# Optimization experiments

Measured on AMD Instinct MI355X. Metric: run time of the kernel, lower is better.

The kernel has to match this reference:

```python
import jax, jax.numpy as jnp
import numpy as np

N, E, D, H, G = 100000, 1600000, 128, 256, 64
N0, N1 = 50000, 25000
SLOPE = 0.01  # PyTorch LeakyReLU default


def lrelu(x):
    return jax.nn.leaky_relu(x, SLOPE)


def seg_sum(x, idx, n):
    return jax.ops.segment_sum(x, idx, num_segments=n)


def seg_max(x, idx, n):
    m = jax.ops.segment_max(x, idx, num_segments=n)
    return jnp.where(jnp.isneginf(m), jnp.zeros_like(m), m)


def mpnn(x, edge_index, edge_attr, w1, b1, g, be, w2, b2):
    # MPNN.forward: add_self_loops -> node MLP -> sym-normalized, edge-weighted scatter-add
    n = x.shape[0]
    ar = jnp.arange(n)
    row = jnp.concatenate([edge_index[0], ar])  # source j (x_j gathered here)
    col = jnp.concatenate([edge_index[1], ar])  # target i (aggregation index)
    ea = jnp.concatenate([edge_attr, jnp.ones((n,), x.dtype)])  # self-loop fill=1.0
    # Linear -> BatchNorm1d(eval: mean0/var1) -> Dropout(eval: id) -> LeakyReLU -> Linear
    h = lrelu((x @ w1.T + b1) * g + be) @ w2.T + b2
    deg = seg_sum(jnp.ones(row.shape, x.dtype), row, n)
    dis = jnp.where(deg > 0, deg ** -0.5, 0.0)
    norm = dis[row] * dis[col]
    msg = (norm * ea)[:, None] * h[row]  # gather + elementwise weighting
    return seg_sum(msg, col, n)          # scatter-add aggregation


def _forward(x, edge_attr, energy, params, edge_index, batch, cluster0, cluster1):
    (w0a, b0a, g0, be0, w0b, b0b,
     w1a, b1a, g1, be1, w1b, b1b,
     w2a, b2a, g2, be2, w2b, b2b,
     emb_w, emb_b, emb_g, emb_be,
     lw1, lb1, lg, lbe, lw2, lb2) = params
    h = mpnn(x, edge_index, edge_attr, w0a, b0a, g0, be0, w0b, b0b) + x
    # --- first graclus max_pool (cluster0 precomputed; edges mapped w/o coalesce) ---
    px = seg_max(lrelu(h), cluster0, N0)
    ox = seg_max(x, cluster0, N0)  # max_pool(origin)
    pe = cluster0[edge_index]
    pb = jnp.maximum(jax.ops.segment_max(batch, cluster0, num_segments=N0), 0)
    # NOTE: mpnn_1 output is assigned to a local `x` and discarded in the original forward,
    # so it does not affect the result; we skip the dead computation.
    h2 = px + ox
    # --- second graclus max_pool ---
    px2 = seg_max(lrelu(h2), cluster1, N1)
    pe2 = cluster1[pe]
    pb2 = jnp.maximum(jax.ops.segment_max(pb, cluster1, num_segments=N1), 0)
    h3 = lrelu(mpnn(px2, pe2, edge_attr, w2a, b2a, g2, be2, w2b, b2b))
    gx = seg_max(h3, pb2, G)  # global_max_pool
    e = lrelu((energy.reshape(G, 21) @ emb_w.T + emb_b) * emb_g + emb_be)
    z = jnp.concatenate([gx, e], axis=1)  # [G, D+8]
    z = lrelu((z @ lw1.T + lb1) * lg + lbe)
    return z @ lw2.T + lb2  # [G, 1]


def setup_inputs() -> dict:
    key = jax.random.key(0)
    ks = iter(jax.random.split(key, 40))

    def lin(k, fo, fi):  # kaiming_normal_ fan_in, leaky_relu
        return jax.random.normal(k, (fo, fi), jnp.float32) * np.float32(np.sqrt(2.0 / fi))

    def bias(n):
        return jnp.full((n,), 0.01, jnp.float32)

    inp = {}
    inp['x'] = jax.random.normal(next(ks), (N, D), jnp.float32)
    inp['edge_attr'] = jax.random.uniform(next(ks), (E,), jnp.float32)
    inp['energy'] = jax.random.normal(next(ks), (G * 21,), jnp.float32)
    # mpnn_0 (D->D->D)
    inp['w0a'] = lin(next(ks), D, D); inp['b0a'] = bias(D)
    inp['g0'] = jnp.ones((D,), jnp.float32); inp['be0'] = jnp.zeros((D,), jnp.float32)
    inp['w0b'] = lin(next(ks), D, D); inp['b0b'] = bias(D)
    # mpnn_1 (D->D->D)  (dead in forward, kept as params)
    inp['w1a'] = lin(next(ks), D, D); inp['b1a'] = bias(D)
    inp['g1'] = jnp.ones((D,), jnp.float32); inp['be1'] = jnp.zeros((D,), jnp.float32)
    inp['w1b'] = lin(next(ks), D, D); inp['b1b'] = bias(D)
    # mpnn_2 (D->H->D)
    inp['w2a'] = lin(next(ks), H, D); inp['b2a'] = bias(H)
    inp['g2'] = jnp.ones((H,), jnp.float32); inp['be2'] = jnp.zeros((H,), jnp.float32)
    inp['w2b'] = lin(next(ks), D, H); inp['b2b'] = bias(D)
    # emb (21->8)
    inp['emb_w'] = lin(next(ks), 8, 21); inp['emb_b'] = bias(8)
    inp['emb_g'] = jnp.ones((8,), jnp.float32); inp['emb_be'] = jnp.zeros((8,), jnp.float32)
    # head ((D+8)->D->1)
    inp['lw1'] = lin(next(ks), D, D + 8); inp['lb1'] = bias(D)
    inp['lg'] = jnp.ones((D,), jnp.float32); inp['lbe'] = jnp.zeros((D,), jnp.float32)
    inp['lw2'] = lin(next(ks), 1, D); inp['lb2'] = bias(1)
    # int inputs
    inp['edge_index'] = jax.random.randint(next(ks), (2, E), 0, N, dtype=jnp.int32)
    inp['batch'] = jnp.sort(jax.random.randint(next(ks), (N,), 0, G, dtype=jnp.int32))
    inp['cluster0'] = jax.random.randint(next(ks), (N,), 0, N0, dtype=jnp.int32)
    inp['cluster1'] = jax.random.randint(next(ks), (N0,), 0, N1, dtype=jnp.int32)
    return inp


def reference(x, edge_attr, energy,
              w0a, b0a, g0, be0, w0b, b0b,
              w1a, b1a, g1, be1, w1b, b1b,
              w2a, b2a, g2, be2, w2b, b2b,
              emb_w, emb_b, emb_g, emb_be,
              lw1, lb1, lg, lbe, lw2, lb2,
              edge_index, batch, cluster0, cluster1):
    params = (w0a, b0a, g0, be0, w0b, b0b,
              w1a, b1a, g1, be1, w1b, b1b,
              w2a, b2a, g2, be2, w2b, b2b,
              emb_w, emb_b, emb_g, emb_be,
              lw1, lb1, lg, lbe, lw2, lb2)
    return _forward(x, edge_attr, energy, params, edge_index, batch, cluster0, cluster1)
```

## Files before the change

### kernel.cpp

```cpp
#include <hip/hip_runtime.h>
#include <math.h>

#define N_NODES 100000
#define N_EDGES 1600000
#define DIM     128
#define NPOOL0  50000
#define NPOOL1  25000
#define NGRAPH  64

typedef __attribute__((ext_vector_type(8))) short short8;
typedef __attribute__((ext_vector_type(4))) float f32x4;

__device__ __forceinline__ float lrelu(float v) { return v > 0.f ? v : 0.01f * v; }

__device__ __forceinline__ unsigned short f2bf(float f) {
    unsigned u = __float_as_uint(f);
    unsigned r = u + 0x7FFFu + ((u >> 16) & 1u);
    return (unsigned short)(r >> 16);
}

__device__ __forceinline__ void atomicMaxF(float* addr, float val) {
    if (val >= 0.f) atomicMax((int*)addr, __float_as_int(val));
    else            atomicMin((unsigned int*)addr, __float_as_uint(val));
}

__global__ __launch_bounds__(256) void init_f(float* __restrict__ deg0, float* __restrict__ deg2,
                                              float* __restrict__ gmax) {
    int i = blockIdx.x * 256 + threadIdx.x;
    if (i < N_NODES) deg0[i] = 1.0f;
    else if (i < N_NODES + NPOOL1) deg2[i - N_NODES] = 1.0f;
    else if (i < N_NODES + NPOOL1 + NGRAPH * DIM) gmax[i - N_NODES - NPOOL1] = -INFINITY;
}
__global__ __launch_bounds__(256) void conv_weights(
        const float* __restrict__ w0a, const float* __restrict__ w0b,
        const float* __restrict__ w2a, const float* __restrict__ w2b,
        unsigned short* __restrict__ o0a, unsigned short* __restrict__ o0b,
        unsigned short* __restrict__ o2a, unsigned short* __restrict__ o2b) {
    int i = blockIdx.x * 256 + threadIdx.x;
    if (i < 16384) o0a[i] = f2bf(w0a[i]);
    else if (i < 32768) o0b[i - 16384] = f2bf(w0b[i - 16384]);
    else if (i < 65536) o2a[i - 32768] = f2bf(w2a[i - 32768]);
    else if (i < 98304) o2b[i - 65536] = f2bf(w2b[i - 65536]);
}

template<int KIN, int HID, bool BF16IN>
__global__ __launch_bounds__(256) void mlp_mfma(
        const void* __restrict__ Xv, int R,
        const unsigned short* __restrict__ W1, const float* __restrict__ B1,
        const float* __restrict__ G1, const float* __restrict__ BE1,
        const unsigned short* __restrict__ W2, const float* __restrict__ B2,
        unsigned short* __restrict__ Y)
{
    constexpr int XS_S = KIN + 8;
    constexpr int TS_S = HID + 8;
    __shared__ unsigned short xs[64 * XS_S];
    __shared__ unsigned short ts[64 * TS_S];

    const int tid = threadIdx.x;
    const int r0 = blockIdx.x * 64;

    {
        const int row = tid >> 2;
        const int c0 = (tid & 3) * 32;
        const int gr = r0 + row;
        if (BF16IN) {
            const unsigned short* X = (const unsigned short*)Xv;
            #pragma unroll
            for (int q = 0; q < 4; ++q) {
                short8 v = short8{0,0,0,0,0,0,0,0};
                if (gr < R) v = *(const short8*)&X[(size_t)gr * KIN + c0 + q * 8];
                *(short8*)&xs[row * XS_S + c0 + q * 8] = v;
            }
        } else {
            const float* X = (const float*)Xv;
            #pragma unroll
            for (int q = 0; q < 4; ++q) {
                short8 v = short8{0,0,0,0,0,0,0,0};
                if (gr < R) {
                    float4 a = *(const float4*)&X[(size_t)gr * KIN + c0 + q * 8];
                    float4 b = *(const float4*)&X[(size_t)gr * KIN + c0 + q * 8 + 4];
                    v[0] = (short)f2bf(a.x); v[1] = (short)f2bf(a.y);
                    v[2] = (short)f2bf(a.z); v[3] = (short)f2bf(a.w);
                    v[4] = (short)f2bf(b.x); v[5] = (short)f2bf(b.y);
                    v[6] = (short)f2bf(b.z); v[7] = (short)f2bf(b.w);
                }
                *(short8*)&xs[row * XS_S + c0 + q * 8] = v;
            }
        }
    }
    __syncthreads();

    const int wv = tid >> 6;
    const int lane = tid & 63;
    const int lr = lane & 15;
    const int lq = lane >> 4;
    const int arow = wv * 16 + lr;

    constexpr int NCG1 = HID / 16;
    constexpr int NK1 = KIN / 32;
    f32x4 acc1[NCG1] = {};
    for (int kc = 0; kc < NK1; ++kc) {
        short8 a = *(short8*)&xs[arow * XS_S + kc * 32 + lq * 8];
        #pragma unroll
        for (int cg = 0; cg < NCG1; ++cg) {
            short8 b = *(const short8*)&W1[(size_t)(cg * 16 + lr) * KIN + kc * 32 + lq * 8];
            acc1[cg] = __builtin_amdgcn_mfma_f32_16x16x32_bf16(a, b, acc1[cg], 0, 0, 0);
        }
    }
    #pragma unroll
    for (int cg = 0; cg < NCG1; ++cg) {
        const int c = cg * 16 + lr;
        const float bb = B1[c], gg = G1[c], ee = BE1[c];
        #pragma unroll
        for (int q = 0; q < 4; ++q) {
            const int rr = wv * 16 + lq * 4 + q;
            float v = (acc1[cg][q] + bb) * gg + ee;
            ts[rr * TS_S + c] = f2bf(lrelu(v));
        }
    }

    constexpr int NK2 = HID / 32;
    f32x4 acc2[8] = {};
    for (int kc = 0; kc < NK2; ++kc) {
        short8 a = *(short8*)&ts[arow * TS_S + kc * 32 + lq * 8];
        #pragma unroll
        for (int cg = 0; cg < 8; ++cg) {
            short8 b = *(const short8*)&W2[(size_t)(cg * 16 + lr) * HID + kc * 32 + lq * 8];
            acc2[cg] = __builtin_amdgcn_mfma_f32_16x16x32_bf16(a, b, acc2[cg], 0, 0, 0);
        }
    }
    #pragma unroll
    for (int cg = 0; cg < 8; ++cg) {
        const int c = cg * 16 + lr;
        const float bb = B2[c];
        #pragma unroll
        for (int q = 0; q < 4; ++q) {
            const int gr = r0 + wv * 16 + lq * 4 + q;
            if (gr < R) Y[(size_t)gr * 128 + c] = f2bf(acc2[cg][q] + bb);
        }
    }
}

__global__ __launch_bounds__(256) void count0(const int* __restrict__ src, const int* __restrict__ dst,
                                              float* __restrict__ deg, int* __restrict__ cnt, int E) {
    int e = blockIdx.x * 256 + threadIdx.x;
    if (e < E) {
        atomicAdd(&deg[src[e]], 1.0f);
        atomicAdd(&cnt[dst[e]], 1);
    }
}
__global__ __launch_bounds__(256) void rsqrt_ip(float* __restrict__ p, int n) {
    int i = blockIdx.x * 256 + threadIdx.x;
    if (i < n) p[i] = rsqrtf(p[i]);
}
__global__ __launch_bounds__(256) void mapnode(
        const int* __restrict__ c0, const int* __restrict__ c1,
        const float* __restrict__ deg0, const int* __restrict__ cnt0,
        int* __restrict__ cmap, float* __restrict__ deg2, int* __restrict__ cnt2, int n) {
    int i = blockIdx.x * 256 + threadIdx.x;
    if (i < n) {
        int m = c1[c0[i]];
        cmap[i] = m;
        float oc = deg0[i] - 1.0f;
        if (oc != 0.f) atomicAdd(&deg2[m], oc);
        int ic = cnt0[i];
        if (ic) atomicAdd(&cnt2[m], ic);
    }
}
__global__ __launch_bounds__(256) void scan_blk(const int* __restrict__ cnt, int* __restrict__ offs,
                                                int* __restrict__ bsum, int n) {
    __shared__ int s[256];
    const int tid = threadIdx.x;
    const int i = blockIdx.x * 256 + tid;
    int v = (i < n) ? cnt[i] : 0;
    s[tid] = v;
    __syncthreads();
    #pragma unroll
    for (int d = 1; d < 256; d <<= 1) {
        int t = (tid >= d) ? s[tid - d] : 0;
        __syncthreads();
        s[tid] += t;
        __syncthreads();
    }
    if (i < n) offs[i] = s[tid] - v;
    if (tid == 255) bsum[blockIdx.x] = s[255];
}
__global__ __launch_bounds__(512) void scan_top(int* __restrict__ bsum, int nb) {
    __shared__ int s[512];
    const int tid = threadIdx.x;
    int v = (tid < nb) ? bsum[tid] : 0;
    s[tid] = v;
    __syncthreads();
    #pragma unroll
    for (int d = 1; d < 512; d <<= 1) {
        int t = (tid >= d) ? s[tid - d] : 0;
        __syncthreads();
        s[tid] += t;
        __syncthreads();
    }
    if (tid < nb) bsum[tid] = s[tid] - v;
}
__global__ __launch_bounds__(256) void scan_add(int* __restrict__ offs, const int* __restrict__ bsum,
                                                int* __restrict__ fill, int n) {
    int i = blockIdx.x * 256 + threadIdx.x;
    if (i < n) {
        int o = offs[i] + bsum[i >> 8];
        offs[i] = o;
        fill[i] = o;
    }
}
__global__ __launch_bounds__(256) void place_pack(const int* __restrict__ dst, const int* __restrict__ srcA,
                                                  const float* __restrict__ ea, const float* __restrict__ dis,
                                                  int* __restrict__ fill, int2* __restrict__ pack, int E) {
    int e = blockIdx.x * 256 + threadIdx.x;
    if (e < E) {
        int d = dst[e];
        int s = srcA[e];
        int pos = atomicAdd(&fill[d], 1);
        pack[pos] = make_int2(s, __float_as_int(dis[s] * ea[e]));
    }
}
__global__ __launch_bounds__(256) void edgemap(
        const int* __restrict__ ei0, const int* __restrict__ ei1,
        const int* __restrict__ cmap,
        int* __restrict__ src2, int* __restrict__ dst2, int E)
{
    int e = blockIdx.x * 256 + threadIdx.x;
    if (e < E) {
        src2[e] = cmap[ei0[e]];
        dst2[e] = cmap[ei1[e]];
    }
}
__global__ __launch_bounds__(256) void seg_count(const int* __restrict__ map, int* __restrict__ cnt, int n) {
    int i = blockIdx.x * 256 + threadIdx.x;
    if (i < n) atomicAdd(&cnt[map[i]], 1);
}
__global__ __launch_bounds__(256) void place_idx(const int* __restrict__ map, int* __restrict__ fill,
                                                 int* __restrict__ list, int n) {
    int i = blockIdx.x * 256 + threadIdx.x;
    if (i < n) {
        int pos = atomicAdd(&fill[map[i]], 1);
        list[pos] = i;
    }
}
__global__ __launch_bounds__(256) void segmax_i32(const int* __restrict__ map, const int* __restrict__ vals,
                                                  int* __restrict__ out, int n) {
    int i = blockIdx.x * 256 + threadIdx.x;
    if (i < n) atomicMax(&out[map[i]], vals[i]);
}

#define EDGE_ITER(K, A0, A1) {                                                  \
    int s_ = __builtin_amdgcn_readlane(pv.x, (K));                              \
    float w_ = __int_as_float(__builtin_amdgcn_readlane(pv.y, (K)));            \
    unsigned hv_ = hrows[(size_t)s_ * 64 + lane];                               \
    float c_ = w_ * di;                                                         \
    A0 += c_ * __uint_as_float(hv_ << 16);                                      \
    A1 += c_ * __uint_as_float(hv_ & 0xFFFF0000u); }

__global__ __launch_bounds__(256) void gather0(
        const unsigned short* __restrict__ h16, const float* __restrict__ x,
        const float* __restrict__ dis, const int* __restrict__ offs,
        const int* __restrict__ cnt, const int2* __restrict__ pack,
        unsigned* __restrict__ agg0)
{
    const int wid = (blockIdx.x * 256 + threadIdx.x) >> 6;
    if (wid >= N_NODES) return;
    const int lane = threadIdx.x & 63;
    const float di = dis[wid];
    const unsigned* hrows = (const unsigned*)h16;

    unsigned hself = hrows[(size_t)wid * 64 + lane];
    float a0 = di * di * __uint_as_float(hself << 16);
    float a1 = di * di * __uint_as_float(hself & 0xFFFF0000u);
    float b0 = 0.f, b1 = 0.f;

    const int base = offs[wid], n = cnt[wid];
    int k0 = 0;
    for (; k0 + 64 <= n; k0 += 64) {
        int2 pv = pack[base + k0 + lane];
        #pragma unroll
        for (int k = 0; k < 64; k += 2) {
            EDGE_ITER(k,     a0, a1);
            EDGE_ITER(k + 1, b0, b1);
        }
    }
    const int rem = n - k0;
    if (rem > 0) {
        int2 pv = (lane < rem) ? pack[base + k0 + lane] : make_int2(0, 0);
        #pragma unroll 4
        for (int k = 0; k < rem; ++k) EDGE_ITER(k, a0, a1);
    }
    a0 += b0; a1 += b1;

    float2 xv = *(const float2*)&x[(size_t)wid * DIM + lane * 2];
    agg0[(size_t)wid * 64 + lane] =
        ((unsigned)f2bf(a1 + xv.y) << 16) | (unsigned)f2bf(a0 + xv.x);
}

__global__ __launch_bounds__(256) void gather2(
        const unsigned short* __restrict__ hm2,
        const float* __restrict__ dis, const int* __restrict__ offs,
        const int* __restrict__ cnt, const int2* __restrict__ pack,
        float* __restrict__ agg2)
{
    const int wid = (blockIdx.x * 256 + threadIdx.x) >> 6;
    if (wid >= NPOOL1) return;
    const int lane = threadIdx.x & 63;
    const float di = dis[wid];
    const unsigned* hrows = (const unsigned*)hm2;

    unsigned hself = hrows[(size_t)wid * 64 + lane];
    float a0 = di * di * __uint_as_float(hself << 16);
    float a1 = di * di * __uint_as_float(hself & 0xFFFF0000u);
    float b0 = 0.f, b1 = 0.f;

    const int base = offs[wid], n = cnt[wid];
    int k0 = 0;
    for (; k0 + 64 <= n; k0 += 64) {
        int2 pv = pack[base + k0 + lane];
        #pragma unroll
        for (int k = 0; k < 64; k += 2) {
            EDGE_ITER(k,     a0, a1);
            EDGE_ITER(k + 1, b0, b1);
        }
    }
    const int rem = n - k0;
    if (rem > 0) {
        int2 pv = (lane < rem) ? pack[base + k0 + lane] : make_int2(0, 0);
        #pragma unroll 4
        for (int k = 0; k < rem; ++k) EDGE_ITER(k, a0, a1);
    }
    a0 += b0; a1 += b1;

    float2 o = make_float2(lrelu(a0), lrelu(a1));
    *(float2*)&agg2[(size_t)wid * DIM + lane * 2] = o;
}

__global__ __launch_bounds__(256) void pool1_gather(
        const unsigned* __restrict__ agg0, const float* __restrict__ x,
        const int* __restrict__ offsc, const int* __restrict__ cntc,
        const int* __restrict__ listc, unsigned* __restrict__ h2)
{
    const int c = (blockIdx.x * 256 + threadIdx.x) >> 6;
    if (c >= NPOOL0) return;
    const int lane = threadIdx.x & 63;
    const int base = offsc[c], n = cntc[c];
    float p0 = -INFINITY, p1 = -INFINITY, o0 = -INFINITY, o1 = -INFINITY;
    for (int k = 0; k < n; ++k) {
        const int node = listc[base + k];
        const unsigned hv = agg0[(size_t)node * 64 + lane];
        const float2 xv = *(const float2*)&x[(size_t)node * 128 + lane * 2];
        p0 = fmaxf(p0, lrelu(__uint_as_float(hv << 16)));
        p1 = fmaxf(p1, lrelu(__uint_as_float(hv & 0xFFFF0000u)));
        o0 = fmaxf(o0, xv.x);
        o1 = fmaxf(o1, xv.y);
    }
    p0 = (p0 == -INFINITY) ? 0.f : p0;
    p1 = (p1 == -INFINITY) ? 0.f : p1;
    o0 = (o0 == -INFINITY) ? 0.f : o0;
    o1 = (o1 == -INFINITY) ? 0.f : o1;
    h2[(size_t)c * 64 + lane] =
        ((unsigned)f2bf(p1 + o1) << 16) | (unsigned)f2bf(p0 + o0);
}

__global__ __launch_bounds__(256) void pool2_gather(
        const unsigned* __restrict__ h2,
        const int* __restrict__ offsd, const int* __restrict__ cntd,
        const int* __restrict__ listd, unsigned* __restrict__ x2)
{
    const int d = (blockIdx.x * 256 + threadIdx.x) >> 6;
    if (d >= NPOOL1) return;
    const int lane = threadIdx.x & 63;
    const int base = offsd[d], n = cntd[d];
    float m0 = -INFINITY, m1 = -INFINITY;
    for (int k = 0; k < n; ++k) {
        const int node = listd[base + k];
        const unsigned hv = h2[(size_t)node * 64 + lane];
        m0 = fmaxf(m0, lrelu(__uint_as_float(hv << 16)));
        m1 = fmaxf(m1, lrelu(__uint_as_float(hv & 0xFFFF0000u)));
    }
    m0 = (m0 == -INFINITY) ? 0.f : m0;
    m1 = (m1 == -INFINITY) ? 0.f : m1;
    x2[(size_t)d * 64 + lane] = ((unsigned)f2bf(m1) << 16) | (unsigned)f2bf(m0);
}

__global__ __launch_bounds__(256) void gpool_scan(
        const float* __restrict__ agg2, const int* __restrict__ listg,
        const int* __restrict__ pb2, float* __restrict__ gmax)
{
    const int wave = (blockIdx.x * 256 + threadIdx.x) >> 6;
    const int lane = threadIdx.x & 63;
    const int CH = (NPOOL1 + 511) / 512;
    const int p0 = wave * CH;
    const int p1 = min(p0 + CH, NPOOL1);
    if (p0 >= NPOOL1) return;

    float m0 = -INFINITY, m1 = -INFINITY;
    int cur = -1;
    for (int p = p0; p < p1; ++p) {
        const int node = listg[p];
        const int g = pb2[node];
        if (g != cur) {
            if (cur >= 0) {
                float* gp = &gmax[(size_t)cur * DIM + lane * 2];
                atomicMaxF(gp + 0, m0);
                atomicMaxF(gp + 1, m1);
            }
            cur = g; m0 = -INFINITY; m1 = -INFINITY;
        }
        const float2 v = *(const float2*)&agg2[(size_t)node * DIM + lane * 2];
        m0 = fmaxf(m0, v.x);
        m1 = fmaxf(m1, v.y);
    }
    float* gp = &gmax[(size_t)cur * DIM + lane * 2];
    atomicMaxF(gp + 0, m0);
    atomicMaxF(gp + 1, m1);
}

__global__ __launch_bounds__(128) void head(
        const float* __restrict__ gmax, const float* __restrict__ energy,
        const float* __restrict__ emb_w, const float* __restrict__ emb_b,
        const float* __restrict__ emb_g, const float* __restrict__ emb_be,
        const float* __restrict__ lw1, const float* __restrict__ lb1,
        const float* __restrict__ lg, const float* __restrict__ lbe,
        const float* __restrict__ lw2, const float* __restrict__ lb2,
        float* __restrict__ out)
{
    const int g = blockIdx.x;
    const int t = threadIdx.x;
    __shared__ float z[136];
    __shared__ float red[128];

    {
        float v = gmax[(size_t)g * DIM + t];
        z[t] = (v == -INFINITY) ? 0.f : v;
    }
    if (t < 8) {
        float s = 0.f;
        #pragma unroll
        for (int k = 0; k < 21; ++k) s += energy[g * 21 + k] * emb_w[t * 21 + k];
        s = (s + emb_b[t]) * emb_g[t] + emb_be[t];
        z[128 + t] = lrelu(s);
    }
    __syncthreads();
    float s = 0.f;
    #pragma unroll 8
    for (int k = 0; k < 136; ++k) s += z[k] * lw1[t * 136 + k];
    float z2 = lrelu((s + lb1[t]) * lg[t] + lbe[t]);
    red[t] = z2 * lw2[t];
    __syncthreads();
    if (t == 0) {
        float acc = lb2[0];
        for (int k = 0; k < 128; ++k) acc += red[k];
        out[g] = acc;
    }
}

extern "C" void kernel_launch(void* const* d_in, const int* in_sizes, int n_in,
                              void* d_out, int out_size, void* d_ws, size_t ws_size,
                              hipStream_t stream) {
    const float* x        = (const float*)d_in[0];
    const float* edge_attr= (const float*)d_in[1];
    const float* energy   = (const float*)d_in[2];
    const float* w0a = (const float*)d_in[3];
    const float* b0a = (const float*)d_in[4];
    const float* g0  = (const float*)d_in[5];
    const float* be0 = (const float*)d_in[6];
    const float* w0b = (const float*)d_in[7];
    const float* b0b = (const float*)d_in[8];
    const float* w2a = (const float*)d_in[15];
    const float* b2a = (const float*)d_in[16];
    const float* g2  = (const float*)d_in[17];
    const float* be2 = (const float*)d_in[18];
    const float* w2b = (const float*)d_in[19];
    const float* b2b = (const float*)d_in[20];
    const float* emb_w  = (const float*)d_in[21];
    const float* emb_b  = (const float*)d_in[22];
    const float* emb_g  = (const float*)d_in[23];
    const float* emb_be = (const float*)d_in[24];
    const float* lw1 = (const float*)d_in[25];
    const float* lb1 = (const float*)d_in[26];
    const float* lg  = (const float*)d_in[27];
    const float* lbe = (const float*)d_in[28];
    const float* lw2 = (const float*)d_in[29];
    const float* lb2 = (const float*)d_in[30];
    const int* ei0   = (const int*)d_in[31];
    const int* ei1   = ei0 + N_EDGES;
    const int* batch = (const int*)d_in[32];
    const int* c0    = (const int*)d_in[33];
    const int* c1    = (const int*)d_in[34];
    float* out = (float*)d_out;

    char* ws = (char*)d_ws;
    unsigned short* h16 = (unsigned short*)(ws + 0);
    int*   src2  = (int*)(ws + 0);
    int*   dst2  = (int*)(ws + 6400000);
    float* agg2  = (float*)(ws + 12800000);
    unsigned* agg0 = (unsigned*)(ws + 25600000);
    unsigned short* hm2 = (unsigned short*)(ws + 25600000);
    int2*  pack0 = (int2*)(ws + 51200000);
    int2*  pack2 = (int2*)(ws + 51200000);
    unsigned* h2 = (unsigned*)(ws + 64000000);
    unsigned* x2 = (unsigned*)(ws + 76800000);
    float* deg0  = (float*)(ws + 83200000);
    float* deg2  = (float*)(ws + 83600000);
    char*  zbase = ws + 83700000;
    int*   cnt0  = (int*)(ws + 83700000);
    int*   cnt2  = (int*)(ws + 84100000);
    int*   cntc  = (int*)(ws + 84200000);
    int*   cntd  = (int*)(ws + 84400000);
    int*   cntg  = (int*)(ws + 84500000);
    int*   pb    = (int*)(ws + 84500256);
    int*   pb2   = (int*)(ws + 84700256);
    const size_t ZBYTES = 84800256 - 83700000;
    int*   offs0 = (int*)(ws + 84800256);
    int*   fill0 = (int*)(ws + 85200256);
    int*   offsc = (int*)(ws + 85600256);
    int*   fillc = (int*)(ws + 85800256);
    int*   listc = (int*)(ws + 86000256);
    int*   offsd = (int*)(ws + 86400256);
    int*   filld = (int*)(ws + 86500256);
    int*   listd = (int*)(ws + 86600256);
    int*   offs2 = (int*)(ws + 86800256);
    int*   fill2 = (int*)(ws + 86900256);
    int*   offsg = (int*)(ws + 87000256);
    int*   fillg = (int*)(ws + 87000512);
    int*   listg = (int*)(ws + 87000768);
    int*   bsum  = (int*)(ws + 87100768);
    int*   cmap  = (int*)(ws + 87103000);
    unsigned short* w0a16 = (unsigned short*)(ws + 87503000);
    unsigned short* w0b16 = (unsigned short*)(ws + 87535768);
    unsigned short* w2a16 = (unsigned short*)(ws + 87568536);
    unsigned short* w2b16 = (unsigned short*)(ws + 87634072);
    float* gmax  = (float*)(ws + 87699608);

    (void)in_sizes; (void)n_in; (void)out_size; (void)ws_size;

    const int NB0 = (N_NODES + 255) / 256;
    const int NBC = (NPOOL0 + 255) / 256;
    const int NB1 = (NPOOL1 + 255) / 256;
    const int NBE = (N_EDGES + 255) / 256;

    hipMemsetAsync(zbase, 0, ZBYTES, stream);
    init_f<<<(N_NODES + NPOOL1 + NGRAPH * DIM + 255) / 256, 256, 0, stream>>>(deg0, deg2, gmax);
    conv_weights<<<384, 256, 0, stream>>>(w0a, w0b, w2a, w2b, w0a16, w0b16, w2a16, w2b16);

    mlp_mfma<128, 128, false><<<(N_NODES + 63) / 64, 256, 0, stream>>>(
        x, N_NODES, w0a16, b0a, g0, be0, w0b16, b0b, h16);
    count0<<<NBE, 256, 0, stream>>>(ei0, ei1, deg0, cnt0, N_EDGES);
    mapnode<<<NB0, 256, 0, stream>>>(c0, c1, deg0, cnt0, cmap, deg2, cnt2, N_NODES);
    rsqrt_ip<<<NB0, 256, 0, stream>>>(deg0, N_NODES);
    scan_blk<<<NB0, 256, 0, stream>>>(cnt0, offs0, bsum, N_NODES);
    scan_top<<<1, 512, 0, stream>>>(bsum, NB0);
    scan_add<<<NB0, 256, 0, stream>>>(offs0, bsum, fill0, N_NODES);
    place_pack<<<NBE, 256, 0, stream>>>(ei1, ei0, edge_attr, deg0, fill0, pack0, N_EDGES);
    gather0<<<(N_NODES * 64) / 256, 256, 0, stream>>>(h16, x, deg0, offs0, cnt0, pack0, agg0);

    seg_count<<<NB0, 256, 0, stream>>>(c0, cntc, N_NODES);
    scan_blk<<<NBC, 256, 0, stream>>>(cntc, offsc, bsum, NPOOL0);
    scan_top<<<1, 512, 0, stream>>>(bsum, NBC);
    scan_add<<<NBC, 256, 0, stream>>>(offsc, bsum, fillc, NPOOL0);
    place_idx<<<NB0, 256, 0, stream>>>(c0, fillc, listc, N_NODES);
    segmax_i32<<<NB0, 256, 0, stream>>>(c0, batch, pb, N_NODES);
    pool1_gather<<<(NPOOL0 * 64) / 256, 256, 0, stream>>>(agg0, x, offsc, cntc, listc, h2);

    seg_count<<<NBC, 256, 0, stream>>>(c1, cntd, NPOOL0);
    scan_blk<<<NB1, 256, 0, stream>>>(cntd, offsd, bsum, NPOOL1);
    scan_top<<<1, 512, 0, stream>>>(bsum, NB1);
    scan_add<<<NB1, 256, 0, stream>>>(offsd, bsum, filld, NPOOL1);
    place_idx<<<NBC, 256, 0, stream>>>(c1, filld, listd, NPOOL0);
    segmax_i32<<<NBC, 256, 0, stream>>>(c1, pb, pb2, NPOOL0);
    pool2_gather<<<(NPOOL1 * 64) / 256, 256, 0, stream>>>(h2, offsd, cntd, listd, x2);

    edgemap<<<NBE, 256, 0, stream>>>(ei0, ei1, cmap, src2, dst2, N_EDGES);
    rsqrt_ip<<<NB1, 256, 0, stream>>>(deg2, NPOOL1);
    scan_blk<<<NB1, 256, 0, stream>>>(cnt2, offs2, bsum, NPOOL1);
    scan_top<<<1, 512, 0, stream>>>(bsum, NB1);
    scan_add<<<NB1, 256, 0, stream>>>(offs2, bsum, fill2, NPOOL1);
    mlp_mfma<128, 256, true><<<(NPOOL1 + 63) / 64, 256, 0, stream>>>(
        x2, NPOOL1, w2a16, b2a, g2, be2, w2b16, b2b, hm2);
    place_pack<<<NBE, 256, 0, stream>>>(dst2, src2, edge_attr, deg2, fill2, pack2, N_EDGES);
    gather2<<<(NPOOL1 * 64) / 256, 256, 0, stream>>>(hm2, deg2, offs2, cnt2, pack2, agg2);

    seg_count<<<NB1, 256, 0, stream>>>(pb2, cntg, NPOOL1);
    scan_blk<<<1, 256, 0, stream>>>(cntg, offsg, bsum, NGRAPH);
    scan_top<<<1, 512, 0, stream>>>(bsum, 1);
    scan_add<<<1, 256, 0, stream>>>(offsg, bsum, fillg, NGRAPH);
    place_idx<<<NB1, 256, 0, stream>>>(pb2, fillg, listg, NPOOL1);
    gpool_scan<<<128, 256, 0, stream>>>(agg2, listg, pb2, gmax);
    head<<<NGRAPH, 128, 0, stream>>>(gmax, energy, emb_w, emb_b, emb_g, emb_be,
                                     lw1, lb1, lg, lbe, lw2, lb2, out);
}
```

Baseline: 1.071 ms.

## Replace global-atomic CSR build with two-pass bucketed counting sort

Degree counting and CSR construction for both message-passing layers now use a two-level radix-style bucket sort. A coarse per-block shared-memory histogram and scatter are followed by a per-bucket shared-memory finalize that computes degrees, offsets and the packed edge list. This replaces the global atomicAdd-heavy count, scan and place kernels. The intent is to cut random global atomic contention and scattered writes, at the cost of more kernel launches, an extra pass over edges, and a serial single-block coarse scan.

```diff
diff --git a/kernel.cpp b/kernel.cpp
--- a/kernel.cpp
+++ b/kernel.cpp
@@ -24,12 +24,9 @@
     else            atomicMin((unsigned int*)addr, __float_as_uint(val));
 }
 
-__global__ __launch_bounds__(256) void init_f(float* __restrict__ deg0, float* __restrict__ deg2,
-                                              float* __restrict__ gmax) {
+__global__ __launch_bounds__(256) void fill_f32(float* __restrict__ p, int n, float v) {
     int i = blockIdx.x * 256 + threadIdx.x;
-    if (i < N_NODES) deg0[i] = 1.0f;
-    else if (i < N_NODES + NPOOL1) deg2[i - N_NODES] = 1.0f;
-    else if (i < N_NODES + NPOOL1 + NGRAPH * DIM) gmax[i - N_NODES - NPOOL1] = -INFINITY;
+    if (i < n) p[i] = v;
 }
 __global__ __launch_bounds__(256) void conv_weights(
         const float* __restrict__ w0a, const float* __restrict__ w0b,
@@ -141,31 +138,145 @@
     }
 }
 
-__global__ __launch_bounds__(256) void count0(const int* __restrict__ src, const int* __restrict__ dst,
-                                              float* __restrict__ deg, int* __restrict__ cnt, int E) {
+template<int SHIFT>
+__global__ __launch_bounds__(256) void hist_coarse(const int* __restrict__ key,
+                                                   int* __restrict__ bh, int E, int nbkt) {
+    __shared__ int h[256];
+    const int t = threadIdx.x;
+    h[t] = 0;
+    __syncthreads();
+    const int base = blockIdx.x * 16384;
+    const int end = min(base + 16384, E);
+    for (int e = base + t; e < end; e += 256) atomicAdd(&h[key[e] >> SHIFT], 1);
+    __syncthreads();
+    if (t < nbkt) bh[t * gridDim.x + blockIdx.x] = h[t];
+}
+__global__ __launch_bounds__(256) void scan_coarse(int* __restrict__ bh, int* __restrict__ bbase,
+                                                   int nblk, int nbkt, int E) {
+    __shared__ int sc[256], tot[256];
+    const int t = threadIdx.x;
+    int sum = 0;
+    if (t < nbkt) {
+        for (int b = 0; b < nblk; ++b) { int v = bh[t * nblk + b]; bh[t * nblk + b] = sum; sum += v; }
+    }
+    tot[t] = sum;
+    sc[t] = sum;
+    __syncthreads();
+    #pragma unroll
+    for (int d = 1; d < 256; d <<= 1) {
+        int v = (t >= d) ? sc[t - d] : 0;
+        __syncthreads();
+        sc[t] += v;
+        __syncthreads();
+    }
+    const int base = sc[t] - tot[t];
+    if (t < nbkt) {
+        for (int b = 0; b < nblk; ++b) bh[t * nblk + b] += base;
+        bbase[t] = base;
+    }
+    if (t == nbkt) bbase[t] = E;
+}
+template<int SHIFT, bool PAY>
+__global__ __launch_bounds__(256) void scatter_coarse(
+        const int* __restrict__ key, const int* __restrict__ aux,
+        const int* __restrict__ bh, int* __restrict__ keyT, int2* __restrict__ packT,
+        int E, int nblk, int nbkt) {
+    __shared__ int off[256];
+    const int t = threadIdx.x;
+    if (t < nbkt) off[t] = bh[t * nblk + blockIdx.x];
+    __syncthreads();
+    const int base = blockIdx.x * 16384;
+    const int end = min(base + 16384, E);
+    for (int e = base + t; e < end; e += 256) {
+        const int k = key[e];
+        const int pos = atomicAdd(&off[k >> SHIFT], 1);
+        keyT[pos] = k;
+        if (PAY) packT[pos] = make_int2(aux[e], e);
+    }
+}
+template<int SHIFT>
+__global__ __launch_bounds__(1 << SHIFT) void hist_finalize(
+        const int* __restrict__ keyT, const int* __restrict__ bbase,
+        float* __restrict__ dis, int nnodes) {
+    constexpr int NB = 1 << SHIFT;
+    __shared__ int h[NB];
+    const int t = threadIdx.x, bkt = blockIdx.x;
+    const int b0 = bbase[bkt], b1 = bbase[bkt + 1];
+    h[t] = 0;
+    __syncthreads();
+    for (int i = b0 + t; i < b1; i += NB) atomicAdd(&h[keyT[i] & (NB - 1)], 1);
+    __syncthreads();
+    const int node = bkt * NB + t;
+    if (node < nnodes) dis[node] = rsqrtf(1.0f + (float)h[t]);
+}
+template<int SHIFT>
+__global__ __launch_bounds__(1 << SHIFT) void bucket_finalize(
+        const int* __restrict__ keyT, const int2* __restrict__ packT,
+        const float* __restrict__ dis, const float* __restrict__ ea,
+        const int* __restrict__ bbase,
+        int* __restrict__ offsN, int* __restrict__ cntN, int2* __restrict__ pack, int nnodes) {
+    constexpr int NB = 1 << SHIFT;
+    __shared__ int h[NB], o[NB];
+    const int t = threadIdx.x, bkt = blockIdx.x;
+    const int b0 = bbase[bkt], b1 = bbase[bkt + 1];
+    h[t] = 0;
+    __syncthreads();
+    for (int i = b0 + t; i < b1; i += NB) atomicAdd(&h[keyT[i] & (NB - 1)], 1);
+    __syncthreads();
+    o[t] = h[t];
+    __syncthreads();
+    #pragma unroll
+    for (int d = 1; d < NB; d <<= 1) {
+        int v = (t >= d) ? o[t - d] : 0;
+        __syncthreads();
+        o[t] += v;
+        __syncthreads();
+    }
+    const int excl = o[t] - h[t];
+    const int node = bkt * NB + t;
+    if (node < nnodes) { offsN[node] = b0 + excl; cntN[node] = h[t]; }
+    o[t] = excl;
+    __syncthreads();
+    for (int i = b0 + t; i < b1; i += NB) {
+        const int k = keyT[i];
+        const int2 p = packT[i];
+        const int pos = b0 + atomicAdd(&o[k & (NB - 1)], 1);
+        pack[pos] = make_int2(p.x, __float_as_int(dis[p.x] * ea[p.y]));
+    }
+}
+
+__global__ __launch_bounds__(256) void build_cmap(const int* __restrict__ c0, const int* __restrict__ c1,
+                                                  int* __restrict__ cmap, int n) {
+    int i = blockIdx.x * 256 + threadIdx.x;
+    if (i < n) cmap[i] = c1[c0[i]];
+}
+__global__ __launch_bounds__(256) void edgemap(
+        const int* __restrict__ ei0, const int* __restrict__ ei1,
+        const int* __restrict__ cmap,
+        int* __restrict__ src2, int* __restrict__ dst2, int E)
+{
     int e = blockIdx.x * 256 + threadIdx.x;
     if (e < E) {
-        atomicAdd(&deg[src[e]], 1.0f);
-        atomicAdd(&cnt[dst[e]], 1);
-    }
-}
-__global__ __launch_bounds__(256) void rsqrt_ip(float* __restrict__ p, int n) {
+        src2[e] = cmap[ei0[e]];
+        dst2[e] = cmap[ei1[e]];
+    }
+}
+__global__ __launch_bounds__(256) void seg_count(const int* __restrict__ map, int* __restrict__ cnt, int n) {
     int i = blockIdx.x * 256 + threadIdx.x;
-    if (i < n) p[i] = rsqrtf(p[i]);
-}
-__global__ __launch_bounds__(256) void mapnode(
-        const int* __restrict__ c0, const int* __restrict__ c1,
-        const float* __restrict__ deg0, const int* __restrict__ cnt0,
-        int* __restrict__ cmap, float* __restrict__ deg2, int* __restrict__ cnt2, int n) {
+    if (i < n) atomicAdd(&cnt[map[i]], 1);
+}
+__global__ __launch_bounds__(256) void place_idx(const int* __restrict__ map, int* __restrict__ fill,
+                                                 int* __restrict__ list, int n) {
     int i = blockIdx.x * 256 + threadIdx.x;
     if (i < n) {
-        int m = c1[c0[i]];
-        cmap[i] = m;
-        float oc = deg0[i] - 1.0f;
-        if (oc != 0.f) atomicAdd(&deg2[m], oc);
-        int ic = cnt0[i];
-        if (ic) atomicAdd(&cnt2[m], ic);
-    }
+        int pos = atomicAdd(&fill[map[i]], 1);
+        list[pos] = i;
+    }
+}
+__global__ __launch_bounds__(256) void segmax_i32(const int* __restrict__ map, const int* __restrict__ vals,
+                                                  int* __restrict__ out, int n) {
+    int i = blockIdx.x * 256 + threadIdx.x;
+    if (i < n) atomicMax(&out[map[i]], vals[i]);
 }
 __global__ __launch_bounds__(256) void scan_blk(const int* __restrict__ cnt, int* __restrict__ offs,
                                                 int* __restrict__ bsum, int n) {
@@ -208,45 +319,6 @@
         offs[i] = o;
         fill[i] = o;
     }
-}
-__global__ __launch_bounds__(256) void place_pack(const int* __restrict__ dst, const int* __restrict__ srcA,
-                                                  const float* __restrict__ ea, const float* __restrict__ dis,
-                                                  int* __restrict__ fill, int2* __restrict__ pack, int E) {
-    int e = blockIdx.x * 256 + threadIdx.x;
-    if (e < E) {
-        int d = dst[e];
-        int s = srcA[e];
-        int pos = atomicAdd(&fill[d], 1);
-        pack[pos] = make_int2(s, __float_as_int(dis[s] * ea[e]));
-    }
-}
-__global__ __launch_bounds__(256) void edgemap(
-        const int* __restrict__ ei0, const int* __restrict__ ei1,
-        const int* __restrict__ cmap,
-        int* __restrict__ src2, int* __restrict__ dst2, int E)
-{
-    int e = blockIdx.x * 256 + threadIdx.x;
-    if (e < E) {
-        src2[e] = cmap[ei0[e]];
-        dst2[e] = cmap[ei1[e]];
-    }
-}
-__global__ __launch_bounds__(256) void seg_count(const int* __restrict__ map, int* __restrict__ cnt, int n) {
-    int i = blockIdx.x * 256 + threadIdx.x;
-    if (i < n) atomicAdd(&cnt[map[i]], 1);
-}
-__global__ __launch_bounds__(256) void place_idx(const int* __restrict__ map, int* __restrict__ fill,
-                                                 int* __restrict__ list, int n) {
-    int i = blockIdx.x * 256 + threadIdx.x;
-    if (i < n) {
-        int pos = atomicAdd(&fill[map[i]], 1);
-        list[pos] = i;
-    }
-}
-__global__ __launch_bounds__(256) void segmax_i32(const int* __restrict__ map, const int* __restrict__ vals,
-                                                  int* __restrict__ out, int n) {
-    int i = blockIdx.x * 256 + threadIdx.x;
-    if (i < n) atomicMax(&out[map[i]], vals[i]);
 }
 
 #define EDGE_ITER(K, A0, A1) {                                                  \
@@ -498,41 +570,42 @@
     float* agg2  = (float*)(ws + 12800000);
     unsigned* agg0 = (unsigned*)(ws + 25600000);
     unsigned short* hm2 = (unsigned short*)(ws + 25600000);
-    int2*  pack0 = (int2*)(ws + 51200000);
-    int2*  pack2 = (int2*)(ws + 51200000);
+    int2*  pack  = (int2*)(ws + 51200000);
     unsigned* h2 = (unsigned*)(ws + 64000000);
+    int2*  packT = (int2*)(ws + 64000000);
     unsigned* x2 = (unsigned*)(ws + 76800000);
-    float* deg0  = (float*)(ws + 83200000);
-    float* deg2  = (float*)(ws + 83600000);
+    int*   keyT  = (int*)(ws + 76800000);
+    float* dis0  = (float*)(ws + 83200000);
+    float* dis2  = (float*)(ws + 83600000);
     char*  zbase = ws + 83700000;
-    int*   cnt0  = (int*)(ws + 83700000);
-    int*   cnt2  = (int*)(ws + 84100000);
-    int*   cntc  = (int*)(ws + 84200000);
-    int*   cntd  = (int*)(ws + 84400000);
-    int*   cntg  = (int*)(ws + 84500000);
-    int*   pb    = (int*)(ws + 84500256);
-    int*   pb2   = (int*)(ws + 84700256);
-    const size_t ZBYTES = 84800256 - 83700000;
-    int*   offs0 = (int*)(ws + 84800256);
-    int*   fill0 = (int*)(ws + 85200256);
-    int*   offsc = (int*)(ws + 85600256);
-    int*   fillc = (int*)(ws + 85800256);
-    int*   listc = (int*)(ws + 86000256);
-    int*   offsd = (int*)(ws + 86400256);
-    int*   filld = (int*)(ws + 86500256);
-    int*   listd = (int*)(ws + 86600256);
-    int*   offs2 = (int*)(ws + 86800256);
-    int*   fill2 = (int*)(ws + 86900256);
-    int*   offsg = (int*)(ws + 87000256);
-    int*   fillg = (int*)(ws + 87000512);
-    int*   listg = (int*)(ws + 87000768);
-    int*   bsum  = (int*)(ws + 87100768);
-    int*   cmap  = (int*)(ws + 87103000);
-    unsigned short* w0a16 = (unsigned short*)(ws + 87503000);
-    unsigned short* w0b16 = (unsigned short*)(ws + 87535768);
-    unsigned short* w2a16 = (unsigned short*)(ws + 87568536);
-    unsigned short* w2b16 = (unsigned short*)(ws + 87634072);
-    float* gmax  = (float*)(ws + 87699608);
+    int*   cntc  = (int*)(ws + 83700000);
+    int*   cntd  = (int*)(ws + 83900000);
+    int*   cntg  = (int*)(ws + 84000000);
+    int*   pb    = (int*)(ws + 84000256);
+    int*   pb2   = (int*)(ws + 84200256);
+    const size_t ZBYTES = 84300256 - 83700000;
+    int*   offsc = (int*)(ws + 84300256);
+    int*   fillc = (int*)(ws + 84500256);
+    int*   listc = (int*)(ws + 84700256);
+    int*   offsd = (int*)(ws + 85100256);
+    int*   filld = (int*)(ws + 85200256);
+    int*   listd = (int*)(ws + 85300256);
+    int*   offsg = (int*)(ws + 85500256);
+    int*   fillg = (int*)(ws + 85500512);
+    int*   listg = (int*)(ws + 85500768);
+    int*   bsum  = (int*)(ws + 85600768);
+    int*   cmap  = (int*)(ws + 85602816);
+    int*   offs0 = (int*)(ws + 86002816);
+    int*   cnt0  = (int*)(ws + 86402816);
+    int*   offs2 = (int*)(ws + 86802816);
+    int*   cnt2  = (int*)(ws + 86902816);
+    unsigned short* w0a16 = (unsigned short*)(ws + 87002816);
+    unsigned short* w0b16 = (unsigned short*)(ws + 87035584);
+    unsigned short* w2a16 = (unsigned short*)(ws + 87068352);
+    unsigned short* w2b16 = (unsigned short*)(ws + 87133888);
+    float* gmax  = (float*)(ws + 87199424);
+    int*   bh    = (int*)(ws + 87232192);
+    int*   bbase = (int*)(ws + 87332544);
 
     (void)in_sizes; (void)n_in; (void)out_size; (void)ws_size;
 
@@ -540,21 +613,27 @@
     const int NBC = (NPOOL0 + 255) / 256;
     const int NB1 = (NPOOL1 + 255) / 256;
     const int NBE = (N_EDGES + 255) / 256;
+    const int NBLK = (N_EDGES + 16383) / 16384;
+    const int NBKT0 = (N_NODES + 511) / 512;
+    const int NBKT2 = (NPOOL1 + 127) / 128;
 
     hipMemsetAsync(zbase, 0, ZBYTES, stream);
-    init_f<<<(N_NODES + NPOOL1 + NGRAPH * DIM + 255) / 256, 256, 0, stream>>>(deg0, deg2, gmax);
+    fill_f32<<<32, 256, 0, stream>>>(gmax, NGRAPH * DIM, -INFINITY);
     conv_weights<<<384, 256, 0, stream>>>(w0a, w0b, w2a, w2b, w0a16, w0b16, w2a16, w2b16);
 
     mlp_mfma<128, 128, false><<<(N_NODES + 63) / 64, 256, 0, stream>>>(
         x, N_NODES, w0a16, b0a, g0, be0, w0b16, b0b, h16);
-    count0<<<NBE, 256, 0, stream>>>(ei0, ei1, deg0, cnt0, N_EDGES);
-    mapnode<<<NB0, 256, 0, stream>>>(c0, c1, deg0, cnt0, cmap, deg2, cnt2, N_NODES);
-    rsqrt_ip<<<NB0, 256, 0, stream>>>(deg0, N_NODES);
-    scan_blk<<<NB0, 256, 0, stream>>>(cnt0, offs0, bsum, N_NODES);
-    scan_top<<<1, 512, 0, stream>>>(bsum, NB0);
-    scan_add<<<NB0, 256, 0, stream>>>(offs0, bsum, fill0, N_NODES);
-    place_pack<<<NBE, 256, 0, stream>>>(ei1, ei0, edge_attr, deg0, fill0, pack0, N_EDGES);
-    gather0<<<(N_NODES * 64) / 256, 256, 0, stream>>>(h16, x, deg0, offs0, cnt0, pack0, agg0);
+
+    hist_coarse<9><<<NBLK, 256, 0, stream>>>(ei0, bh, N_EDGES, NBKT0);
+    scan_coarse<<<1, 256, 0, stream>>>(bh, bbase, NBLK, NBKT0, N_EDGES);
+    scatter_coarse<9, false><<<NBLK, 256, 0, stream>>>(ei0, nullptr, bh, keyT, nullptr, N_EDGES, NBLK, NBKT0);
+    hist_finalize<9><<<NBKT0, 512, 0, stream>>>(keyT, bbase, dis0, N_NODES);
+
+    hist_coarse<9><<<NBLK, 256, 0, stream>>>(ei1, bh, N_EDGES, NBKT0);
+    scan_coarse<<<1, 256, 0, stream>>>(bh, bbase, NBLK, NBKT0, N_EDGES);
+    scatter_coarse<9, true><<<NBLK, 256, 0, stream>>>(ei1, ei0, bh, keyT, packT, N_EDGES, NBLK, NBKT0);
+    bucket_finalize<9><<<NBKT0, 512, 0, stream>>>(keyT, packT, dis0, edge_attr, bbase, offs0, cnt0, pack, N_NODES);
+    gather0<<<(N_NODES * 64) / 256, 256, 0, stream>>>(h16, x, dis0, offs0, cnt0, pack, agg0);
 
     seg_count<<<NB0, 256, 0, stream>>>(c0, cntc, N_NODES);
     scan_blk<<<NBC, 256, 0, stream>>>(cntc, offsc, bsum, NPOOL0);
@@ -572,15 +651,21 @@
     segmax_i32<<<NBC, 256, 0, stream>>>(c1, pb, pb2, NPOOL0);
     pool2_gather<<<(NPOOL1 * 64) / 256, 256, 0, stream>>>(h2, offsd, cntd, listd, x2);
 
+    build_cmap<<<NB0, 256, 0, stream>>>(c0, c1, cmap, N_NODES);
     edgemap<<<NBE, 256, 0, stream>>>(ei0, ei1, cmap, src2, dst2, N_EDGES);
-    rsqrt_ip<<<NB1, 256, 0, stream>>>(deg2, NPOOL1);
-    scan_blk<<<NB1, 256, 0, stream>>>(cnt2, offs2, bsum, NPOOL1);
-    scan_top<<<1, 512, 0, stream>>>(bsum, NB1);
-    scan_add<<<NB1, 256, 0, stream>>>(offs2, bsum, fill2, NPOOL1);
     mlp_mfma<128, 256, true><<<(NPOOL1 + 63) / 64, 256, 0, stream>>>(
         x2, NPOOL1, w2a16, b2a, g2, be2, w2b16, b2b, hm2);
-    place_pack<<<NBE, 256, 0, stream>>>(dst2, src2, edge_attr, deg2, fill2, pack2, N_EDGES);
-    gather2<<<(NPOOL1 * 64) / 256, 256, 0, stream>>>(hm2, deg2, offs2, cnt2, pack2, agg2);
+
+    hist_coarse<7><<<NBLK, 256, 0, stream>>>(src2, bh, N_EDGES, NBKT2);
+    scan_coarse<<<1, 256, 0, stream>>>(bh, bbase, NBLK, NBKT2, N_EDGES);
+    scatter_coarse<7, false><<<NBLK, 256, 0, stream>>>(src2, nullptr, bh, keyT, nullptr, N_EDGES, NBLK, NBKT2);
+    hist_finalize<7><<<NBKT2, 128, 0, stream>>>(keyT, bbase, dis2, NPOOL1);
+
+    hist_coarse<7><<<NBLK, 256, 0, stream>>>(dst2, bh, N_EDGES, NBKT2);
+    scan_coarse<<<1, 256, 0, stream>>>(bh, bbase, NBLK, NBKT2, N_EDGES);
+    scatter_coarse<7, true><<<NBLK, 256, 0, stream>>>(dst2, src2, bh, keyT, packT, N_EDGES, NBLK, NBKT2);
+    bucket_finalize<7><<<NBKT2, 128, 0, stream>>>(keyT, packT, dis2, edge_attr, bbase, offs2, cnt2, pack, NPOOL1);
+    gather2<<<(NPOOL1 * 64) / 256, 256, 0, stream>>>(hm2, dis2, offs2, cnt2, pack, agg2);
 
     seg_count<<<NB1, 256, 0, stream>>>(pb2, cntg, NPOOL1);
     scan_blk<<<1, 256, 0, stream>>>(cntg, offsg, bsum, NGRAPH);
```

New measurement: 1.250 ms. 1.17x slower.
